# Kernel optimization log

Measured on AMD Instinct MI355X. Metric: run time of the kernel, lower is better.

Reference implementation:

```python
import jax, jax.numpy as jnp
import numpy as np
import math

D, H, F = 1024, 16, 4096
DH = D // H
EPS_LN = 1e-5


def _layernorm(x, scale, bias):
    mu = jnp.mean(x, axis=-1, keepdims=True)
    var = jnp.mean(jnp.square(x - mu), axis=-1, keepdims=True)
    return (x - mu) * jax.lax.rsqrt(var + EPS_LN) * scale + bias


def setup_inputs() -> dict:
    key = jax.random.key(0)
    ks = jax.random.split(key, 16)
    B, T = 2, 2048
    src = jax.random.normal(ks[0], (B, T, D), dtype=jnp.float32)
    attn_mask = jax.random.randint(ks[1], (T, T), 0, 2) == 1  # bool [T,S], True = masked
    xavier = lambda k, shp: jax.random.uniform(k, shp, jnp.float32, -1.0, 1.0) * math.sqrt(6.0 / (shp[0] + shp[1]))
    return {
        "src": src, "attn_mask": attn_mask,
        "q_w": xavier(ks[2], (D, D)), "q_b": jnp.zeros((D,), jnp.float32),
        "k_w": xavier(ks[3], (D, D)), "k_b": jnp.zeros((D,), jnp.float32),
        "v_w": xavier(ks[4], (D, D)), "v_b": jnp.zeros((D,), jnp.float32),
        "o_w": xavier(ks[5], (D, D)), "o_b": jnp.zeros((D,), jnp.float32),
        "l1_w": xavier(ks[6], (F, D)), "l1_b": jnp.zeros((F,), jnp.float32),
        "l2_w": xavier(ks[7], (D, F)), "l2_b": jnp.zeros((D,), jnp.float32),
        "n1_s": jnp.ones((D,), jnp.float32), "n1_b": jnp.zeros((D,), jnp.float32),
        "n2_s": jnp.ones((D,), jnp.float32), "n2_b": jnp.zeros((D,), jnp.float32),
        "alpha_attn": jax.random.normal(ks[8], (), jnp.float32) * 0.1,
        "alpha_ff": jax.random.normal(ks[9], (), jnp.float32) * 0.1,
    }


def reference(src, attn_mask, q_w, q_b, k_w, k_b, v_w, v_b, o_w, o_b,
              l1_w, l1_b, l2_w, l2_b, n1_s, n1_b, n2_s, n2_b,
              alpha_attn, alpha_ff):
    B, T, _ = src.shape
    # --- self-attention block (post-norm layer, dropout=0 => identity) ---
    q = (src @ q_w.T + q_b).reshape(B, T, H, DH).transpose(0, 2, 1, 3)  # [B,H,T,DH]
    k = (src @ k_w.T + k_b).reshape(B, T, H, DH).transpose(0, 2, 1, 3)
    v = (src @ v_w.T + v_b).reshape(B, T, H, DH).transpose(0, 2, 1, 3)
    scores = jnp.einsum('bhtd,bhsd->bhts', q, k) / math.sqrt(DH)  # [B,H,T,S]
    scores = jnp.where(attn_mask[None, None, :, :], -jnp.inf, scores)
    probs = jax.nn.softmax(scores + 1e-9, axis=-1)
    probs = jnp.where(jnp.isinf(scores), 0.0, probs)  # zero where masked (custom semantics)
    attn = jnp.einsum('bhts,bhsd->bhtd', probs, v).transpose(0, 2, 1, 3).reshape(B, T, D)
    attn = attn @ o_w.T + o_b
    x = _layernorm(src + alpha_attn * attn, n1_s, n1_b)
    # --- FFN block ---
    ff = jax.nn.relu(x @ l1_w.T + l1_b) @ l2_w.T + l2_b
    x = _layernorm(x + alpha_ff * ff, n2_s, n2_b)
    return x
```

## Files before the change

### kernel.cpp

```cpp
#include <hip/hip_runtime.h>
#include <math.h>

#define Dm 1024
#define Hh 16
#define DHd 64
#define Ff 4096
#define Tt 2048
#define Bb 2

#define ATT_C2 0.18033688011112042f

typedef __bf16 bf16_8 __attribute__((ext_vector_type(8)));
typedef __bf16 bf16x2 __attribute__((ext_vector_type(2)));
typedef __bf16 bf16x4 __attribute__((ext_vector_type(4)));
typedef float  f32x4  __attribute__((ext_vector_type(4)));

__device__ __forceinline__ unsigned short f2bf(float f) {
    unsigned int u = __float_as_uint(f);
    unsigned int r = (u + 0x7fffu + ((u >> 16) & 1u)) >> 16;
    return (unsigned short)r;
}

__device__ __forceinline__ bf16x2 pkbf(float a, float b) {
#if __has_builtin(__builtin_amdgcn_cvt_pk_bf16_f32)
    return __builtin_amdgcn_cvt_pk_bf16_f32(a, b);
#else
    bf16x2 r; r[0] = (__bf16)a; r[1] = (__bf16)b; return r;
#endif
}
__device__ __forceinline__ bf16x4 pkbf4(float a, float b, float c, float d) {
    bf16x2 lo = pkbf(a, b), hi = pkbf(c, d);
    return __builtin_shufflevector(lo, hi, 0, 1, 2, 3);
}

__device__ __forceinline__ void gld_lds16(const void* g, void* l) {
    __builtin_amdgcn_global_load_lds(
        (const __attribute__((address_space(1))) void*)g,
        (__attribute__((address_space(3))) void*)l,
        16, 0, 0);
}

__global__ __launch_bounds__(256) void preprocess_kernel(
    const float* __restrict__ q_w, const float* __restrict__ k_w,
    const float* __restrict__ v_w, const float* __restrict__ o_w,
    const float* __restrict__ l1_w, const float* __restrict__ l2_w,
    const float* __restrict__ src, const int* __restrict__ mask,
    const float* __restrict__ q_b, const float* __restrict__ k_b,
    unsigned short* __restrict__ qkw, unsigned short* __restrict__ vw16,
    unsigned short* __restrict__ ow,  unsigned short* __restrict__ l1w,
    unsigned short* __restrict__ l2w, unsigned short* __restrict__ srcb,
    unsigned* __restrict__ mbit, float* __restrict__ qkb)
{
    const int bid = blockIdx.x;
    const int tid = threadIdx.x;
    if (bid < 16384) {
        int i = bid * 256 + tid;
        const float* sp; unsigned short* dp; int off;
        if (i < 1048576) {
            if (i < 262144)      { sp = q_w; dp = qkw;           off = i; }
            else if (i < 524288) { sp = k_w; dp = qkw + 1048576; off = i - 262144; }
            else if (i < 786432) { sp = v_w; dp = vw16;          off = i - 524288; }
            else                 { sp = o_w; dp = ow;            off = i - 786432; }
        } else if (i < 2097152)  { sp = l1_w; dp = l1w;          off = i - 1048576; }
        else if (i < 3145728)    { sp = l2_w; dp = l2w;          off = i - 2097152; }
        else                     { sp = src;  dp = srcb;         off = i - 3145728; }
        float4 v = ((const float4*)sp)[off];
        ((bf16x4*)dp)[off] = pkbf4(v.x, v.y, v.z, v.w);
    } else if (bid < 16896) {
        int w = (bid - 16384) * 256 + tid;
        const int* p = mask + (size_t)w * 32;
        unsigned bits = 0;
        #pragma unroll
        for (int j = 0; j < 8; ++j) {
            int4 v = ((const int4*)p)[j];
            bits |= (v.x != 0 ? 1u : 0u) << (j * 4 + 0);
            bits |= (v.y != 0 ? 1u : 0u) << (j * 4 + 1);
            bits |= (v.z != 0 ? 1u : 0u) << (j * 4 + 2);
            bits |= (v.w != 0 ? 1u : 0u) << (j * 4 + 3);
        }
        mbit[w] = bits;
    } else {
        int i = (bid - 16896) * 256 + tid;
        qkb[i] = (i < 1024) ? q_b[i] : k_b[i - 1024];
    }
}

template<int RELU, int BF16OUT>
__global__ __launch_bounds__(256) void gemm_bf16_kernel(
    const unsigned short* __restrict__ A, const unsigned short* __restrict__ W,
    const float* __restrict__ bias, void* __restrict__ C, void* __restrict__ C2,
    int M, int N, int K, int ldc, int ksub)
{
    __shared__ __bf16 As[128][64];
    __shared__ __bf16 Bs[128][64];
    const int tid  = threadIdx.x;
    const int lane = tid & 63;
    const int wave = tid >> 6;
    const int m0 = blockIdx.y * 128;
    const int n0 = blockIdx.x * 128;
    const int lr8 = lane >> 3;
    const int gch = (lane & 7) ^ lr8;
    const int wm = (wave & 1) * 64;
    const int wn = (wave >> 1) * 64;
    const int quad = lane >> 4;
    const int lm = lane & 15;
    const int z  = blockIdx.z;
    const int kstart = z * ksub;
    void* Cz = (z == 0) ? C : C2;

    f32x4 acc[4][4];
    #pragma unroll
    for (int i = 0; i < 4; i++)
        #pragma unroll
        for (int j = 0; j < 4; j++) {
            acc[i][j][0] = 0.f; acc[i][j][1] = 0.f;
            acc[i][j][2] = 0.f; acc[i][j][3] = 0.f;
        }

    for (int k0 = kstart; k0 < kstart + ksub; k0 += 64) {
        __syncthreads();
        #pragma unroll
        for (int i = 0; i < 4; i++) {
            int seg = wave * 4 + i;
            int r = seg * 8 + lr8;
            gld_lds16(A + (size_t)(m0 + r) * K + k0 + gch * 8, &As[seg * 8][0]);
            gld_lds16(W + (size_t)(n0 + r) * K + k0 + gch * 8, &Bs[seg * 8][0]);
        }
        __syncthreads();
        #pragma unroll
        for (int kh = 0; kh < 2; kh++) {
            bf16_8 af[4], bfr[4];
            #pragma unroll
            for (int t = 0; t < 4; t++) {
                int ch = (kh * 4 + quad) ^ (lm & 7);
                af[t]  = *(const bf16_8*)&As[wm + t * 16 + lm][ch * 8];
                bfr[t] = *(const bf16_8*)&Bs[wn + t * 16 + lm][ch * 8];
            }
            #pragma unroll
            for (int i = 0; i < 4; i++)
                #pragma unroll
                for (int j = 0; j < 4; j++)
                    acc[i][j] = __builtin_amdgcn_mfma_f32_16x16x32_bf16(
                        af[i], bfr[j], acc[i][j], 0, 0, 0);
        }
    }

    float bvc[4];
    #pragma unroll
    for (int j = 0; j < 4; j++)
        bvc[j] = (z == 0) ? bias[n0 + wn + j * 16 + lm] : 0.f;

    #pragma unroll
    for (int i = 0; i < 4; i++)
        #pragma unroll
        for (int j = 0; j < 4; j++) {
            int col = n0 + wn + j * 16 + lm;
            #pragma unroll
            for (int r = 0; r < 4; r++) {
                int row = m0 + wm + i * 16 + quad * 4 + r;
                float v = acc[i][j][r] + bvc[j];
                if (RELU) v = fmaxf(v, 0.f);
                if (BF16OUT)
                    ((unsigned short*)Cz)[(size_t)row * ldc + col] = f2bf(v);
                else
                    ((float*)Cz)[(size_t)row * ldc + col] = v;
            }
        }
}

__global__ __launch_bounds__(256, 2) void gemm_ffn1_kernel(
    const unsigned short* __restrict__ A, const unsigned short* __restrict__ W,
    const float* __restrict__ bias, unsigned short* __restrict__ C)
{
    __shared__ __bf16 As[256][64];
    __shared__ __bf16 Bs[128][64];
    const int tid  = threadIdx.x;
    const int lane = tid & 63;
    const int wave = tid >> 6;
    const int m0 = blockIdx.y * 256;
    const int n0 = blockIdx.x * 128;
    const int lr8 = lane >> 3;
    const int gch = (lane & 7) ^ lr8;
    const int quad = lane >> 4;
    const int lm = lane & 15;

    f32x4 acc[4][8];
    #pragma unroll
    for (int i = 0; i < 4; i++)
        #pragma unroll
        for (int j = 0; j < 8; j++) {
            acc[i][j][0] = 0.f; acc[i][j][1] = 0.f;
            acc[i][j][2] = 0.f; acc[i][j][3] = 0.f;
        }

    for (int k0 = 0; k0 < 1024; k0 += 64) {
        __syncthreads();
        #pragma unroll
        for (int i = 0; i < 8; i++) {
            int seg = wave * 8 + i;
            int r = seg * 8 + lr8;
            gld_lds16(A + (size_t)(m0 + r) * 1024 + k0 + gch * 8, &As[seg * 8][0]);
        }
        #pragma unroll
        for (int i = 0; i < 4; i++) {
            int seg = wave * 4 + i;
            int r = seg * 8 + lr8;
            gld_lds16(W + (size_t)(n0 + r) * 1024 + k0 + gch * 8, &Bs[seg * 8][0]);
        }
        __syncthreads();
        #pragma unroll
        for (int kh = 0; kh < 2; kh++) {
            const int ch = (kh * 4 + quad) ^ (lm & 7);
            bf16_8 af[4], bfr[8];
            #pragma unroll
            for (int t = 0; t < 4; t++)
                af[t] = *(const bf16_8*)&As[wave * 64 + t * 16 + lm][ch * 8];
            #pragma unroll
            for (int j = 0; j < 8; j++)
                bfr[j] = *(const bf16_8*)&Bs[j * 16 + lm][ch * 8];
            #pragma unroll
            for (int i = 0; i < 4; i++)
                #pragma unroll
                for (int j = 0; j < 8; j++)
                    acc[i][j] = __builtin_amdgcn_mfma_f32_16x16x32_bf16(
                        af[i], bfr[j], acc[i][j], 0, 0, 0);
        }
    }

    float bv[8];
    #pragma unroll
    for (int j = 0; j < 8; j++) bv[j] = bias[n0 + j * 16 + lm];

    #pragma unroll
    for (int i = 0; i < 4; i++)
        #pragma unroll
        for (int j = 0; j < 8; j++) {
            int col = n0 + j * 16 + lm;
            #pragma unroll
            for (int r = 0; r < 4; r++) {
                int row = m0 + wave * 64 + i * 16 + quad * 4 + r;
                float v = fmaxf(acc[i][j][r] + bv[j], 0.f);
                C[(size_t)row * Ff + col] = f2bf(v);
            }
        }
}

__global__ __launch_bounds__(256) void gemm_qkvt_kernel(
    const unsigned short* __restrict__ srcb, const unsigned short* __restrict__ qkw,
    const unsigned short* __restrict__ vw16, const float* __restrict__ qkb,
    const float* __restrict__ v_b,
    unsigned short* __restrict__ qk16, unsigned short* __restrict__ vtf)
{
    const int bid = blockIdx.x;
    const unsigned short *A, *W;
    const float* bias;
    unsigned short* C;
    int m0, n0, ldc;
    bool qscale, rowbias;
    if (bid < 512) {
        A = srcb; W = qkw; bias = qkb; C = qk16;
        n0 = (bid & 15) * 128; m0 = (bid >> 4) * 128;
        ldc = 2048; qscale = true; rowbias = false;
    } else {
        int b2 = bid - 512;
        A = vw16; W = srcb; bias = v_b; C = vtf;
        n0 = (b2 & 31) * 128; m0 = (b2 >> 5) * 128;
        ldc = 4096; qscale = false; rowbias = true;
    }
    const int K = 1024;

    __shared__ __bf16 As[128][64];
    __shared__ __bf16 Bs[128][64];
    const int tid  = threadIdx.x;
    const int lane = tid & 63;
    const int wave = tid >> 6;
    const int lr8 = lane >> 3;
    const int gch = (lane & 7) ^ lr8;
    const int wm = (wave & 1) * 64;
    const int wn = (wave >> 1) * 64;
    const int quad = lane >> 4;
    const int lm = lane & 15;

    f32x4 acc[4][4];
    #pragma unroll
    for (int i = 0; i < 4; i++)
        #pragma unroll
        for (int j = 0; j < 4; j++) {
            acc[i][j][0] = 0.f; acc[i][j][1] = 0.f;
            acc[i][j][2] = 0.f; acc[i][j][3] = 0.f;
        }

    for (int k0 = 0; k0 < K; k0 += 64) {
        __syncthreads();
        #pragma unroll
        for (int i = 0; i < 4; i++) {
            int seg = wave * 4 + i;
            int r = seg * 8 + lr8;
            gld_lds16(A + (size_t)(m0 + r) * K + k0 + gch * 8, &As[seg * 8][0]);
            gld_lds16(W + (size_t)(n0 + r) * K + k0 + gch * 8, &Bs[seg * 8][0]);
        }
        __syncthreads();
        #pragma unroll
        for (int kh = 0; kh < 2; kh++) {
            bf16_8 af[4], bfr[4];
            #pragma unroll
            for (int t = 0; t < 4; t++) {
                int ch = (kh * 4 + quad) ^ (lm & 7);
                af[t]  = *(const bf16_8*)&As[wm + t * 16 + lm][ch * 8];
                bfr[t] = *(const bf16_8*)&Bs[wn + t * 16 + lm][ch * 8];
            }
            #pragma unroll
            for (int i = 0; i < 4; i++)
                #pragma unroll
                for (int j = 0; j < 4; j++)
                    acc[i][j] = __builtin_amdgcn_mfma_f32_16x16x32_bf16(
                        af[i], bfr[j], acc[i][j], 0, 0, 0);
        }
    }

    float bvc[4];
    float brr[4][4];
    if (!rowbias) {
        #pragma unroll
        for (int j = 0; j < 4; j++) bvc[j] = bias[n0 + wn + j * 16 + lm];
    } else {
        #pragma unroll
        for (int i = 0; i < 4; i++) {
            float4 t4 = *(const float4*)&bias[m0 + wm + i * 16 + quad * 4];
            brr[i][0] = t4.x; brr[i][1] = t4.y; brr[i][2] = t4.z; brr[i][3] = t4.w;
        }
    }

    #pragma unroll
    for (int i = 0; i < 4; i++)
        #pragma unroll
        for (int j = 0; j < 4; j++) {
            int col = n0 + wn + j * 16 + lm;
            #pragma unroll
            for (int r = 0; r < 4; r++) {
                int row = m0 + wm + i * 16 + quad * 4 + r;
                float v = acc[i][j][r] + (rowbias ? brr[i][r] : bvc[j]);
                if (qscale && col < 1024) v *= ATT_C2;
                C[(size_t)row * ldc + col] = f2bf(v);
            }
        }
}

__global__ __launch_bounds__(512, 4) void attn_mfma_kernel(
    const unsigned short* __restrict__ qk,
    const unsigned short* __restrict__ vt,
    const unsigned* __restrict__ mb,
    unsigned short* __restrict__ out)
{
    __shared__ __bf16 Ks[128 * 64];
    __shared__ __bf16 Vt[64 * 128];
    __shared__ __bf16 Ps[8][16 * 64];

    const int tid  = threadIdx.x;
    const int lane = tid & 63;
    const int wave = tid >> 6;
    const int c    = lane & 15;
    const int quad = lane >> 4;
    const int bh = blockIdx.y;
    const int b = bh >> 4, h = bh & 15;
    const int t0 = blockIdx.x * 128;
    const int tw = t0 + wave * 16;

    bf16_8 qf[2];
    #pragma unroll
    for (int ks = 0; ks < 2; ++ks)
        qf[ks] = *(const bf16_8*)(qk +
            (size_t)(b * Tt + tw + c) * 2048 +
            h * DHd + quad * 8 + ks * 32);

    f32x4 oacc[4];
    f32x4 ol;
    ol[0] = 0.f; ol[1] = 0.f; ol[2] = 0.f; ol[3] = 0.f;
    #pragma unroll
    for (int dt = 0; dt < 4; ++dt) {
        oacc[dt][0] = 0.f; oacc[dt][1] = 0.f;
        oacc[dt][2] = 0.f; oacc[dt][3] = 0.f;
    }
    bf16_8 vone;
    {
        __bf16 one = (__bf16)1.0f;
        #pragma unroll
        for (int j = 0; j < 8; ++j) vone[j] = one;
    }

    const int krow8 = lane >> 3;
    const int kj    = (lane & 7) ^ krow8;
    const int vr4   = lane >> 4;

    for (int st16 = 0; st16 < 16; ++st16) {
        const int s0 = st16 * 128;
        __syncthreads();

        #pragma unroll
        for (int i = 0; i < 2; ++i) {
            int ci = wave * 2 + i;
            {
                int r = 8 * ci + krow8;
                const unsigned short* g = qk +
                    (size_t)(b * Tt + s0 + r) * 2048 + 1024 + h * DHd + kj * 8;
                gld_lds16(g, &Ks[ci * 512]);
            }
            {
                int d = 4 * ci + vr4;
                int jj = (lane & 15) ^ (d & 7);
                const unsigned short* g = vt +
                    (size_t)(h * DHd + d) * 4096 + b * Tt + s0 + jj * 8;
                gld_lds16(g, &Vt[ci * 512]);
            }
        }

        unsigned mwv[4];
        #pragma unroll
        for (int sp = 0; sp < 4; ++sp)
            mwv[sp] = mb[(size_t)(tw + c) * 64 + (s0 >> 5) + sp];

        __syncthreads();

        #pragma unroll
        for (int half = 0; half < 2; ++half) {
            #pragma unroll
            for (int s8l = 0; s8l < 4; ++s8l) {
                const int s8 = half * 4 + s8l;
                bf16_8 kf0 = *(const bf16_8*)&Ks[((s8 * 16 + c) * 8 + ((quad + 0) ^ (c & 7))) * 8];
                bf16_8 kf1 = *(const bf16_8*)&Ks[((s8 * 16 + c) * 8 + ((quad + 4) ^ (c & 7))) * 8];
                f32x4 zr; zr[0] = 0.f; zr[1] = 0.f; zr[2] = 0.f; zr[3] = 0.f;
                zr = __builtin_amdgcn_mfma_f32_16x16x32_bf16(kf0, qf[0], zr, 0, 0, 0);
                f32x4 sv = __builtin_amdgcn_mfma_f32_16x16x32_bf16(kf1, qf[1], zr, 0, 0, 0);
                unsigned mword = mwv[s8 >> 1];
                int bp = (s8 & 1) * 16 + quad * 4;
                float p[4];
                #pragma unroll
                for (int r = 0; r < 4; ++r) {
                    int bit = (mword >> (bp + r)) & 1;
                    float x = bit ? -1e30f : sv[r];
                    p[r] = __builtin_amdgcn_exp2f(x);
                }
                bf16x4 pk4v = pkbf4(p[0], p[1], p[2], p[3]);
                int ch = (s8l * 2 + (quad >> 1)) ^ (c & 7);
                *(bf16x4*)&Ps[wave][c * 64 + ch * 8 + (quad & 1) * 4] = pk4v;
            }
            #pragma unroll
            for (int ks = 0; ks < 2; ++ks) {
                bf16_8 pa, vf[4];
                {
                    int ch = (ks * 4 + quad) ^ (c & 7);
                    pa = *(const bf16_8*)&Ps[wave][c * 64 + ch * 8];
                }
                #pragma unroll
                for (int dt = 0; dt < 4; ++dt) {
                    int sc = half * 8 + ks * 4 + quad;
                    int d = dt * 16 + c;
                    vf[dt] = *(const bf16_8*)&Vt[(d * 16 + (sc ^ (c & 7))) * 8];
                }
                #pragma unroll
                for (int dt = 0; dt < 4; ++dt)
                    oacc[dt] = __builtin_amdgcn_mfma_f32_16x16x32_bf16(
                        pa, vf[dt], oacc[dt], 0, 0, 0);
                ol = __builtin_amdgcn_mfma_f32_16x16x32_bf16(
                    pa, vone, ol, 0, 0, 0);
            }
        }
    }

    #pragma unroll
    for (int r = 0; r < 4; ++r) {
        float l = ol[r];
        float inv = (l > 0.f) ? 1.f / l : 0.f;
        int row = b * Tt + tw + quad * 4 + r;
        #pragma unroll
        for (int dt = 0; dt < 4; ++dt)
            out[(size_t)row * Dm + h * DHd + dt * 16 + c] =
                f2bf(oacc[dt][r] * inv);
    }
}

template<int NPARTS, int BASEBF, int OUTF32, int OUTBF>
__global__ __launch_bounds__(256) void residual_ln_kernel(
    const void* __restrict__ base, const float* __restrict__ d0,
    const float* __restrict__ d1,
    const float* __restrict__ alpha_p, const float* __restrict__ scale,
    const float* __restrict__ bias, float* __restrict__ out,
    unsigned short* __restrict__ out_bf)
{
    const int row = blockIdx.x;
    const int tid = threadIdx.x;
    const float alpha = alpha_p[0];
    float4 xb;
    if (BASEBF) {
        bf16x4 bb = ((const bf16x4*)((const unsigned short*)base + (size_t)row * Dm))[tid];
        xb.x = (float)bb[0]; xb.y = (float)bb[1]; xb.z = (float)bb[2]; xb.w = (float)bb[3];
    } else {
        xb = ((const float4*)((const float*)base + (size_t)row * Dm))[tid];
    }
    float4 xd = ((const float4*)(d0 + (size_t)row * Dm))[tid];
    if (NPARTS == 2) {
        float4 x2 = ((const float4*)(d1 + (size_t)row * Dm))[tid];
        xd.x += x2.x; xd.y += x2.y; xd.z += x2.z; xd.w += x2.w;
    }
    float4 x;
    x.x = xb.x + alpha * xd.x;
    x.y = xb.y + alpha * xd.y;
    x.z = xb.z + alpha * xd.z;
    x.w = xb.w + alpha * xd.w;
    float s  = x.x + x.y + x.z + x.w;
    float sq = x.x*x.x + x.y*x.y + x.z*x.z + x.w*x.w;
    #pragma unroll
    for (int off = 32; off > 0; off >>= 1) {
        s  += __shfl_down(s, off, 64);
        sq += __shfl_down(sq, off, 64);
    }
    __shared__ float red[8];
    const int w = tid >> 6;
    if ((tid & 63) == 0) { red[w] = s; red[4 + w] = sq; }
    __syncthreads();
    s  = red[0] + red[1] + red[2] + red[3];
    sq = red[4] + red[5] + red[6] + red[7];
    const float mu  = s * (1.f / Dm);
    const float var = sq * (1.f / Dm) - mu * mu;
    const float r   = rsqrtf(var + 1e-5f);
    float4 sc = ((const float4*)scale)[tid];
    float4 bi = ((const float4*)bias)[tid];
    float4 o;
    o.x = (x.x - mu) * r * sc.x + bi.x;
    o.y = (x.y - mu) * r * sc.y + bi.y;
    o.z = (x.z - mu) * r * sc.z + bi.z;
    o.w = (x.w - mu) * r * sc.w + bi.w;
    if (OUTF32)
        ((float4*)(out + (size_t)row * Dm))[tid] = o;
    if (OUTBF)
        ((bf16x4*)(out_bf + (size_t)row * Dm))[tid] = pkbf4(o.x, o.y, o.z, o.w);
}

extern "C" void kernel_launch(void* const* d_in, const int* in_sizes, int n_in,
                              void* d_out, int out_size, void* d_ws, size_t ws_size,
                              hipStream_t stream)
{
    (void)in_sizes; (void)n_in; (void)out_size; (void)ws_size;
    const float* src  = (const float*)d_in[0];
    const int*   mask = (const int*)  d_in[1];
    const float* q_w  = (const float*)d_in[2];
    const float* q_b  = (const float*)d_in[3];
    const float* k_w  = (const float*)d_in[4];
    const float* k_b  = (const float*)d_in[5];
    const float* v_w  = (const float*)d_in[6];
    const float* v_b  = (const float*)d_in[7];
    const float* o_w  = (const float*)d_in[8];
    const float* o_b  = (const float*)d_in[9];
    const float* l1_w = (const float*)d_in[10];
    const float* l1_b = (const float*)d_in[11];
    const float* l2_w = (const float*)d_in[12];
    const float* l2_b = (const float*)d_in[13];
    const float* n1_s = (const float*)d_in[14];
    const float* n1_b = (const float*)d_in[15];
    const float* n2_s = (const float*)d_in[16];
    const float* n2_b = (const float*)d_in[17];
    const float* a_attn = (const float*)d_in[18];
    const float* a_ff   = (const float*)d_in[19];

    const size_t MB = 1024 * 1024;
    char* w = (char*)d_ws;
    unsigned short* qkw  = (unsigned short*)(w + 0);
    unsigned short* vw16 = (unsigned short*)(w + 4  * MB);
    unsigned short* ow   = (unsigned short*)(w + 6  * MB);
    unsigned short* l1w  = (unsigned short*)(w + 8  * MB);
    unsigned short* l2w  = (unsigned short*)(w + 16 * MB);
    unsigned short* srcb = (unsigned short*)(w + 24 * MB);
    unsigned short* qk16 = (unsigned short*)(w + 32 * MB);
    unsigned short* vtf  = (unsigned short*)(w + 48 * MB);
    unsigned*       mbit = (unsigned*)      (w + 56 * MB);
    float*          qkb  = (float*)         (w + 56 * MB + 524288);
    unsigned short* atb  = (unsigned short*)(w + 24 * MB);
    float*          o0   = (float*)         (w + 58 * MB);
    float*          o1   = (float*)         (w + 74 * MB);
    unsigned short* x1b  = (unsigned short*)(w + 48 * MB);
    unsigned short* hb   = (unsigned short*)(w + 58 * MB);
    float*          fp0  = (float*)         (w + 0);
    float*          fp1  = (float*)         (w + 32 * MB);

    const int MR = Bb * Tt;
    dim3 blk(256);

    preprocess_kernel<<<dim3(16904), blk, 0, stream>>>(
        q_w, k_w, v_w, o_w, l1_w, l2_w, src, mask, q_b, k_b,
        qkw, vw16, ow, l1w, l2w, srcb, mbit, qkb);
    gemm_qkvt_kernel<<<dim3(768), blk, 0, stream>>>(
        srcb, qkw, vw16, qkb, v_b, qk16, vtf);
    attn_mfma_kernel<<<dim3(16, 32), dim3(512), 0, stream>>>(qk16, vtf, mbit, atb);
    gemm_bf16_kernel<0, 0><<<dim3(8, 32, 2), blk, 0, stream>>>(
        atb, ow, o_b, o0, o1, MR, Dm, Dm, Dm, 512);
    residual_ln_kernel<2, 0, 0, 1><<<dim3(MR), blk, 0, stream>>>(
        src, o0, o1, a_attn, n1_s, n1_b, nullptr, x1b);
    gemm_ffn1_kernel<<<dim3(32, 16), blk, 0, stream>>>(x1b, l1w, l1_b, hb);
    gemm_bf16_kernel<0, 0><<<dim3(8, 32, 2), blk, 0, stream>>>(
        hb, l2w, l2_b, fp0, fp1, MR, Dm, Ff, Dm, Ff / 2);
    residual_ln_kernel<2, 1, 1, 0><<<dim3(MR), blk, 0, stream>>>(
        x1b, fp0, fp1, a_ff, n2_s, n2_b, (float*)d_out, nullptr);
}
```

Baseline: 377.1 us.

## Rework attention kernel to 32x32 MFMA with register P and double-buffered K/V

Rewrites the attention kernel so each of 4 waves handles 32 query rows using 32x32x16 bf16 MFMAs instead of 16x16x32. The softmax probabilities now stay in registers and are rearranged with permlane32 swaps, replacing the LDS round trip through Ps. The row sums are accumulated in scalar registers, replacing the extra MFMA against a vector of ones. K/V tiles are double-buffered so the next tile's global-to-LDS load overlaps compute on the current one, which also removes one barrier per iteration. The block shrinks to 256 threads with more LDS per block, which may change occupancy.

```diff
diff --git a/kernel.cpp b/kernel.cpp
--- a/kernel.cpp
+++ b/kernel.cpp
@@ -14,6 +14,8 @@
 typedef __bf16 bf16x2 __attribute__((ext_vector_type(2)));
 typedef __bf16 bf16x4 __attribute__((ext_vector_type(4)));
 typedef float  f32x4  __attribute__((ext_vector_type(4)));
+typedef float  f32x16 __attribute__((ext_vector_type(16)));
+typedef unsigned int u32x4 __attribute__((ext_vector_type(4)));
 
 __device__ __forceinline__ unsigned short f2bf(float f) {
     unsigned int u = __float_as_uint(f);
@@ -31,6 +33,15 @@
 __device__ __forceinline__ bf16x4 pkbf4(float a, float b, float c, float d) {
     bf16x2 lo = pkbf(a, b), hi = pkbf(c, d);
     return __builtin_shufflevector(lo, hi, 0, 1, 2, 3);
+}
+
+__device__ __forceinline__ void plswap32(unsigned &a, unsigned &b) {
+#if __has_builtin(__builtin_amdgcn_permlane32_swap)
+    auto r = __builtin_amdgcn_permlane32_swap((int)a, (int)b, false, false);
+    a = (unsigned)r[0]; b = (unsigned)r[1];
+#else
+    asm volatile("v_permlane32_swap_b32 %0, %1" : "+v"(a), "+v"(b));
+#endif
 }
 
 __device__ __forceinline__ void gld_lds16(const void* g, void* l) {
@@ -346,137 +357,148 @@
         }
 }
 
-__global__ __launch_bounds__(512, 4) void attn_mfma_kernel(
+__global__ __launch_bounds__(256) void attn_mfma_kernel(
     const unsigned short* __restrict__ qk,
     const unsigned short* __restrict__ vt,
     const unsigned* __restrict__ mb,
     unsigned short* __restrict__ out)
 {
-    __shared__ __bf16 Ks[128 * 64];
-    __shared__ __bf16 Vt[64 * 128];
-    __shared__ __bf16 Ps[8][16 * 64];
+    __shared__ __bf16 Ks[2][128 * 64];
+    __shared__ __bf16 Vt[2][64 * 128];
+    __shared__ float  l_s[128];
 
     const int tid  = threadIdx.x;
     const int lane = tid & 63;
     const int wave = tid >> 6;
-    const int c    = lane & 15;
-    const int quad = lane >> 4;
+    const int l31  = lane & 31;
+    const int hi   = lane >> 5;
+    const int x7   = l31 & 7;
     const int bh = blockIdx.y;
     const int b = bh >> 4, h = bh & 15;
-    const int t0 = blockIdx.x * 128;
-    const int tw = t0 + wave * 16;
-
-    bf16_8 qf[2];
-    #pragma unroll
-    for (int ks = 0; ks < 2; ++ks)
-        qf[ks] = *(const bf16_8*)(qk +
-            (size_t)(b * Tt + tw + c) * 2048 +
-            h * DHd + quad * 8 + ks * 32);
-
-    f32x4 oacc[4];
-    f32x4 ol;
-    ol[0] = 0.f; ol[1] = 0.f; ol[2] = 0.f; ol[3] = 0.f;
-    #pragma unroll
-    for (int dt = 0; dt < 4; ++dt) {
-        oacc[dt][0] = 0.f; oacc[dt][1] = 0.f;
-        oacc[dt][2] = 0.f; oacc[dt][3] = 0.f;
-    }
-    bf16_8 vone;
-    {
-        __bf16 one = (__bf16)1.0f;
-        #pragma unroll
-        for (int j = 0; j < 8; ++j) vone[j] = one;
-    }
+    const int tw = blockIdx.x * 128 + wave * 32;
+
+    bf16_8 qf[4];
+    #pragma unroll
+    for (int ds4 = 0; ds4 < 4; ++ds4)
+        qf[ds4] = *(const bf16_8*)(qk +
+            (size_t)(b * Tt + tw + l31) * 2048 + h * DHd + ds4 * 16 + hi * 8);
+
+    f32x16 oacc[2];
+    #pragma unroll
+    for (int d = 0; d < 2; ++d)
+        #pragma unroll
+        for (int r = 0; r < 16; ++r) oacc[d][r] = 0.f;
+    float lsum = 0.f;
 
     const int krow8 = lane >> 3;
     const int kj    = (lane & 7) ^ krow8;
     const int vr4   = lane >> 4;
 
-    for (int st16 = 0; st16 < 16; ++st16) {
-        const int s0 = st16 * 128;
-        __syncthreads();
-
-        #pragma unroll
-        for (int i = 0; i < 2; ++i) {
-            int ci = wave * 2 + i;
+    auto STAGE = [&](int nb, int s0) {
+        #pragma unroll
+        for (int i = 0; i < 4; ++i) {
+            int ci = wave * 4 + i;
             {
                 int r = 8 * ci + krow8;
                 const unsigned short* g = qk +
                     (size_t)(b * Tt + s0 + r) * 2048 + 1024 + h * DHd + kj * 8;
-                gld_lds16(g, &Ks[ci * 512]);
+                gld_lds16(g, &Ks[nb][ci * 512]);
             }
             {
                 int d = 4 * ci + vr4;
                 int jj = (lane & 15) ^ (d & 7);
                 const unsigned short* g = vt +
                     (size_t)(h * DHd + d) * 4096 + b * Tt + s0 + jj * 8;
-                gld_lds16(g, &Vt[ci * 512]);
-            }
-        }
+                gld_lds16(g, &Vt[nb][ci * 512]);
+            }
+        }
+    };
+
+    STAGE(0, 0);
+
+    for (int st = 0; st < 16; ++st) {
+        const int cb = st & 1;
+        const int s0 = st * 128;
+        __syncthreads();
 
         unsigned mwv[4];
         #pragma unroll
-        for (int sp = 0; sp < 4; ++sp)
-            mwv[sp] = mb[(size_t)(tw + c) * 64 + (s0 >> 5) + sp];
-
-        __syncthreads();
-
-        #pragma unroll
-        for (int half = 0; half < 2; ++half) {
-            #pragma unroll
-            for (int s8l = 0; s8l < 4; ++s8l) {
-                const int s8 = half * 4 + s8l;
-                bf16_8 kf0 = *(const bf16_8*)&Ks[((s8 * 16 + c) * 8 + ((quad + 0) ^ (c & 7))) * 8];
-                bf16_8 kf1 = *(const bf16_8*)&Ks[((s8 * 16 + c) * 8 + ((quad + 4) ^ (c & 7))) * 8];
-                f32x4 zr; zr[0] = 0.f; zr[1] = 0.f; zr[2] = 0.f; zr[3] = 0.f;
-                zr = __builtin_amdgcn_mfma_f32_16x16x32_bf16(kf0, qf[0], zr, 0, 0, 0);
-                f32x4 sv = __builtin_amdgcn_mfma_f32_16x16x32_bf16(kf1, qf[1], zr, 0, 0, 0);
-                unsigned mword = mwv[s8 >> 1];
-                int bp = (s8 & 1) * 16 + quad * 4;
-                float p[4];
+        for (int sb = 0; sb < 4; ++sb)
+            mwv[sb] = mb[(size_t)(tw + l31) * 64 + (s0 >> 5) + sb];
+
+        if (st < 15) STAGE(cb ^ 1, s0 + 128);
+
+        #pragma unroll
+        for (int sb = 0; sb < 4; ++sb) {
+            f32x16 sacc;
+            #pragma unroll
+            for (int r = 0; r < 16; ++r) sacc[r] = 0.f;
+            #pragma unroll
+            for (int ds4 = 0; ds4 < 4; ++ds4) {
+                bf16_8 kf = *(const bf16_8*)&Ks[cb][
+                    (sb * 32 + l31) * 64 + (((ds4 * 2 + hi) ^ x7) * 8)];
+                sacc = __builtin_amdgcn_mfma_f32_32x32x16_bf16(
+                    kf, qf[ds4], sacc, 0, 0, 0);
+            }
+            const unsigned mword = mwv[sb];
+            float p[16];
+            #pragma unroll
+            for (int g = 0; g < 4; ++g)
                 #pragma unroll
-                for (int r = 0; r < 4; ++r) {
-                    int bit = (mword >> (bp + r)) & 1;
-                    float x = bit ? -1e30f : sv[r];
-                    p[r] = __builtin_amdgcn_exp2f(x);
+                for (int m = 0; m < 4; ++m) {
+                    const int reg = g * 4 + m;
+                    const int srow = m + 8 * g + 4 * hi;
+                    float x = ((mword >> srow) & 1u) ? -1e30f : sacc[reg];
+                    float e = __builtin_amdgcn_exp2f(x);
+                    p[reg] = e;
+                    lsum += e;
                 }
-                bf16x4 pk4v = pkbf4(p[0], p[1], p[2], p[3]);
-                int ch = (s8l * 2 + (quad >> 1)) ^ (c & 7);
-                *(bf16x4*)&Ps[wave][c * 64 + ch * 8 + (quad & 1) * 4] = pk4v;
-            }
-            #pragma unroll
-            for (int ks = 0; ks < 2; ++ks) {
-                bf16_8 pa, vf[4];
-                {
-                    int ch = (ks * 4 + quad) ^ (c & 7);
-                    pa = *(const bf16_8*)&Ps[wave][c * 64 + ch * 8];
+            unsigned u[4], v[4];
+            #pragma unroll
+            for (int g = 0; g < 4; ++g) {
+                u[g] = __builtin_bit_cast(unsigned, pkbf(p[g * 4 + 0], p[g * 4 + 1]));
+                v[g] = __builtin_bit_cast(unsigned, pkbf(p[g * 4 + 2], p[g * 4 + 3]));
+            }
+            plswap32(u[0], u[1]); plswap32(v[0], v[1]);
+            plswap32(u[2], u[3]); plswap32(v[2], v[3]);
+            u32x4 w0; w0[0] = u[0]; w0[1] = v[0]; w0[2] = u[1]; w0[3] = v[1];
+            u32x4 w1; w1[0] = u[2]; w1[1] = v[2]; w1[2] = u[3]; w1[3] = v[3];
+            bf16_8 pa0 = __builtin_bit_cast(bf16_8, w0);
+            bf16_8 pa1 = __builtin_bit_cast(bf16_8, w1);
+            #pragma unroll
+            for (int kst = 0; kst < 2; ++kst) {
+                bf16_8 pa = kst ? pa1 : pa0;
+                #pragma unroll
+                for (int dblk = 0; dblk < 2; ++dblk) {
+                    int cpos = (sb * 4 + kst * 2 + hi) ^ x7;
+                    bf16_8 vf = *(const bf16_8*)&Vt[cb][
+                        ((dblk * 32 + l31) * 16 + cpos) * 8];
+                    oacc[dblk] = __builtin_amdgcn_mfma_f32_32x32x16_bf16(
+                        pa, vf, oacc[dblk], 0, 0, 0);
                 }
-                #pragma unroll
-                for (int dt = 0; dt < 4; ++dt) {
-                    int sc = half * 8 + ks * 4 + quad;
-                    int d = dt * 16 + c;
-                    vf[dt] = *(const bf16_8*)&Vt[(d * 16 + (sc ^ (c & 7))) * 8];
-                }
-                #pragma unroll
-                for (int dt = 0; dt < 4; ++dt)
-                    oacc[dt] = __builtin_amdgcn_mfma_f32_16x16x32_bf16(
-                        pa, vf[dt], oacc[dt], 0, 0, 0);
-                ol = __builtin_amdgcn_mfma_f32_16x16x32_bf16(
-                    pa, vone, ol, 0, 0, 0);
-            }
-        }
-    }
-
-    #pragma unroll
-    for (int r = 0; r < 4; ++r) {
-        float l = ol[r];
-        float inv = (l > 0.f) ? 1.f / l : 0.f;
-        int row = b * Tt + tw + quad * 4 + r;
-        #pragma unroll
-        for (int dt = 0; dt < 4; ++dt)
-            out[(size_t)row * Dm + h * DHd + dt * 16 + c] =
-                f2bf(oacc[dt][r] * inv);
-    }
+            }
+        }
+    }
+
+    unsigned la = __builtin_bit_cast(unsigned, lsum), lb = la;
+    plswap32(la, lb);
+    float ltot = __builtin_bit_cast(float, la) + __builtin_bit_cast(float, lb);
+    l_s[wave * 32 + l31] = (ltot > 0.f) ? 1.f / ltot : 0.f;
+    __syncthreads();
+
+    #pragma unroll
+    for (int g = 0; g < 4; ++g)
+        #pragma unroll
+        for (int m = 0; m < 4; ++m) {
+            const int reg = g * 4 + m;
+            const int tr = m + 8 * g + 4 * hi;
+            float inv = l_s[wave * 32 + tr];
+            int row = b * Tt + tw + tr;
+            #pragma unroll
+            for (int dblk = 0; dblk < 2; ++dblk)
+                out[(size_t)row * Dm + h * DHd + dblk * 32 + l31] =
+                    f2bf(oacc[dblk][reg] * inv);
+        }
 }
 
 template<int NPARTS, int BASEBF, int OUTF32, int OUTBF>
@@ -590,7 +612,7 @@
         qkw, vw16, ow, l1w, l2w, srcb, mbit, qkb);
     gemm_qkvt_kernel<<<dim3(768), blk, 0, stream>>>(
         srcb, qkw, vw16, qkb, v_b, qk16, vtf);
-    attn_mfma_kernel<<<dim3(16, 32), dim3(512), 0, stream>>>(qk16, vtf, mbit, atb);
+    attn_mfma_kernel<<<dim3(16, 32), blk, 0, stream>>>(qk16, vtf, mbit, atb);
     gemm_bf16_kernel<0, 0><<<dim3(8, 32, 2), blk, 0, stream>>>(
         atb, ow, o_b, o0, o1, MR, Dm, Dm, Dm, 512);
     residual_ln_kernel<2, 0, 0, 1><<<dim3(MR), blk, 0, stream>>>(
```

After: 370.3 us. No clear change (-1.8%).
